# Kernel tuning notes

Measured on AMD Instinct MI355X. Metric: run time of the kernel, lower is better.

## Reference

```python
import jax, jax.numpy as jnp
import numpy as np

D_MODEL = 1024
NHEAD = 16
HEAD_DIM = D_MODEL // NHEAD
D_FF = 4096
B, S = 2, 2048
LN_EPS = 1e-5


def _linear_params(key, d_out, d_in):
    kw, kb = jax.random.split(key)
    lim = 1.0 / np.sqrt(d_in)
    W = jax.random.uniform(kw, (d_out, d_in), jnp.float32, -lim, lim)
    b = jax.random.uniform(kb, (d_out,), jnp.float32, -lim, lim)
    return W, b


def setup_inputs() -> dict:
    key = jax.random.key(0)
    ks = jax.random.split(key, 8)
    src = jax.random.normal(ks[0], (B, S, D_MODEL), jnp.float32)
    mask = jax.random.randint(ks[1], (B, S), 0, 2).astype(bool)
    Wq, bq = _linear_params(ks[2], D_MODEL, D_MODEL)
    Wk, bk = _linear_params(ks[3], D_MODEL, D_MODEL)
    Wv, bv = _linear_params(ks[4], D_MODEL, D_MODEL)
    Wo, bo = _linear_params(ks[5], D_MODEL, D_MODEL)
    W1, b1 = _linear_params(ks[6], D_FF, D_MODEL)
    W2, b2 = _linear_params(ks[7], D_MODEL, D_FF)
    ln1_g = jnp.ones((D_MODEL,), jnp.float32)
    ln1_b = jnp.zeros((D_MODEL,), jnp.float32)
    ln2_g = jnp.ones((D_MODEL,), jnp.float32)
    ln2_b = jnp.zeros((D_MODEL,), jnp.float32)
    return dict(src=src, mask=mask, Wq=Wq, bq=bq, Wk=Wk, bk=bk, Wv=Wv, bv=bv,
                Wo=Wo, bo=bo, W1=W1, b1=b1, W2=W2, b2=b2,
                ln1_g=ln1_g, ln1_b=ln1_b, ln2_g=ln2_g, ln2_b=ln2_b)


def _layernorm(x, g, b):
    mu = jnp.mean(x, axis=-1, keepdims=True)
    var = jnp.mean(jnp.square(x - mu), axis=-1, keepdims=True)
    return (x - mu) * jax.lax.rsqrt(var + LN_EPS) * g + b


def reference(src, mask, Wq, bq, Wk, bk, Wv, bv, Wo, bo, W1, b1, W2, b2,
              ln1_g, ln1_b, ln2_g, ln2_b):
    batch, seq, _ = src.shape
    src_norm = _layernorm(src, ln1_g, ln1_b)
    # projections (torch Linear: x @ W.T + b), split heads -> [B,H,S,Dh]
    def proj(W, b):
        y = jnp.einsum('bsi,oi->bso', src_norm, W) + b
        return y.reshape(batch, seq, NHEAD, HEAD_DIM).transpose(0, 2, 1, 3)
    q, k, v = proj(Wq, bq), proj(Wk, bk), proj(Wv, bv)
    scores = jnp.einsum('bhqd,bhkd->bhqk', q, k) / np.sqrt(HEAD_DIM)
    scores = jnp.where(mask[:, None, None, :], -10000.0, scores)
    attn_probs = jax.nn.softmax(scores, axis=-1)
    attn_out = jnp.einsum('bhqk,bhkd->bhqd', attn_probs, v)
    attn_out = attn_out.transpose(0, 2, 1, 3).reshape(batch, seq, D_MODEL)
    attn_out = jnp.einsum('bsi,oi->bso', attn_out, Wo) + bo
    src = src + attn_out
    src_norm2 = _layernorm(src, ln2_g, ln2_b)
    h = jax.nn.relu(jnp.einsum('bsi,oi->bso', src_norm2, W1) + b1)
    ff = jnp.einsum('bsi,oi->bso', h, W2) + b2
    src = src + ff
    return (src, attn_probs)
```

## Files before the change

### kernel.cpp

```cpp
#include <hip/hip_runtime.h>
#include <math.h>

typedef __bf16 bf16;
typedef __bf16 bf16x4 __attribute__((ext_vector_type(4)));
typedef __bf16 bf16x8 __attribute__((ext_vector_type(8)));
typedef float f32x4 __attribute__((ext_vector_type(4)));

__device__ __forceinline__ f32x4 mfma16(bf16x8 a, bf16x8 b, f32x4 c) {
  return __builtin_amdgcn_mfma_f32_16x16x32_bf16(a, b, c, 0, 0, 0);
}

__device__ __forceinline__ void gload_lds16(const void* g, void* l) {
  __builtin_amdgcn_global_load_lds((__attribute__((address_space(1))) void*)(g),
                                   (__attribute__((address_space(3))) void*)(l),
                                   16, 0, 0);
}

__global__ __launch_bounds__(256)
void cvt_all(const float* __restrict__ Wq, const float* __restrict__ Wk,
             const float* __restrict__ Wv, const float* __restrict__ Wo,
             const float* __restrict__ W1, const float* __restrict__ W2,
             const float* __restrict__ bq, const float* __restrict__ bk,
             const float* __restrict__ bv, bf16* __restrict__ wqkv,
             bf16* __restrict__ wob, bf16* __restrict__ w1b,
             bf16* __restrict__ w2b, float* __restrict__ bqkv) {
  const int i = blockIdx.x * 256 + threadIdx.x;
  if (i < 3145728) {
    float4 v;
    bf16* dst;
    size_t di;
    if (i < 262144) { v = ((const float4*)Wq)[i]; dst = wqkv; di = i; }
    else if (i < 524288) { v = ((const float4*)Wk)[i - 262144]; dst = wqkv; di = i; }
    else if (i < 786432) { v = ((const float4*)Wv)[i - 524288]; dst = wqkv; di = i; }
    else if (i < 1048576) { v = ((const float4*)Wo)[i - 786432]; dst = wob; di = i - 786432; }
    else if (i < 2097152) { v = ((const float4*)W1)[i - 1048576]; dst = w1b; di = i - 1048576; }
    else { v = ((const float4*)W2)[i - 2097152]; dst = w2b; di = i - 2097152; }
    bf16x4 o;
    o[0] = (bf16)v.x; o[1] = (bf16)v.y; o[2] = (bf16)v.z; o[3] = (bf16)v.w;
    reinterpret_cast<bf16x4*>(dst)[di] = o;
  } else {
    const int j = i - 3145728;
    const float* s = (j < 256) ? bq : ((j < 512) ? bk : bv);
    reinterpret_cast<float4*>(bqkv)[j] = reinterpret_cast<const float4*>(s)[j & 255];
  }
}

__global__ __launch_bounds__(256)
void ln_bf16(const float* __restrict__ x, const float* __restrict__ g,
             const float* __restrict__ bta, bf16* __restrict__ y) {
  const int row = blockIdx.x, t = threadIdx.x;
  const float4 v = reinterpret_cast<const float4*>(x)[(size_t)row * 256 + t];
  float s1 = v.x + v.y + v.z + v.w;
  float s2 = v.x * v.x + v.y * v.y + v.z * v.z + v.w * v.w;
#pragma unroll
  for (int m = 1; m < 64; m <<= 1) {
    s1 += __shfl_xor(s1, m);
    s2 += __shfl_xor(s2, m);
  }
  __shared__ float red[8];
  if ((t & 63) == 0) { red[(t >> 6) * 2] = s1; red[(t >> 6) * 2 + 1] = s2; }
  __syncthreads();
  s1 = red[0] + red[2] + red[4] + red[6];
  s2 = red[1] + red[3] + red[5] + red[7];
  const float mu = s1 * (1.f / 1024.f);
  const float rs = rsqrtf(s2 * (1.f / 1024.f) - mu * mu + 1e-5f);
  const float4 gv = reinterpret_cast<const float4*>(g)[t];
  const float4 bv = reinterpret_cast<const float4*>(bta)[t];
  bf16x4 o;
  o[0] = (bf16)((v.x - mu) * rs * gv.x + bv.x);
  o[1] = (bf16)((v.y - mu) * rs * gv.y + bv.y);
  o[2] = (bf16)((v.z - mu) * rs * gv.z + bv.z);
  o[3] = (bf16)((v.w - mu) * rs * gv.w + bv.w);
  reinterpret_cast<bf16x4*>(y)[(size_t)row * 256 + t] = o;
}

__global__ __launch_bounds__(256)
void tr_v(const bf16* __restrict__ QKV, bf16* __restrict__ VT) {
  __shared__ bf16 T[64 * 80];
  const int t = threadIdx.x;
  const int sb = blockIdx.x * 64, h = blockIdx.y, b = blockIdx.z;
  const int srow = t >> 2, c16 = t & 3;
  const bf16* src = QKV + (size_t)(b * 2048 + sb + srow) * 3072 + 2048 + h * 64 + c16 * 16;
  bf16x8 a0 = *reinterpret_cast<const bf16x8*>(src);
  bf16x8 a1 = *reinterpret_cast<const bf16x8*>(src + 8);
  *reinterpret_cast<bf16x8*>(&T[srow * 80 + c16 * 16]) = a0;
  *reinterpret_cast<bf16x8*>(&T[srow * 80 + c16 * 16 + 8]) = a1;
  __syncthreads();
  const int drow = t >> 2, sq = t & 3;
  bf16x8 o0, o1;
#pragma unroll
  for (int j = 0; j < 8; ++j) o0[j] = T[(sq * 16 + j) * 80 + drow];
#pragma unroll
  for (int j = 0; j < 8; ++j) o1[j] = T[(sq * 16 + 8 + j) * 80 + drow];
  bf16* dst = VT + ((size_t)(b * 16 + h) * 64 + drow) * 2048 + sb + sq * 16;
  *reinterpret_cast<bf16x8*>(dst) = o0;
  *reinterpret_cast<bf16x8*>(dst + 8) = o1;
}

template <bool OUT_BF16, bool RELU, bool RES, bool QSC>
__global__ __launch_bounds__(256)
void gemm_bt(const bf16* __restrict__ A, const bf16* __restrict__ Bw,
             const float* __restrict__ bias, const float* __restrict__ res,
             void* __restrict__ Cout, int M, int N, int K) {
  __shared__ bf16 As[2][128 * 32];
  __shared__ bf16 Bs[2][128 * 32];
  const int t = threadIdx.x, wave = t >> 6, lane = t & 63;
  const int l15 = lane & 15, lhi = lane >> 4;
  const int nwg = gridDim.x * gridDim.y;
  const int orig = blockIdx.y * gridDim.x + blockIdx.x;
  const int wgid = (orig & 7) * (nwg >> 3) + (orig >> 3);
  const int bx = wgid % gridDim.x, by = wgid / gridDim.x;
  const int m0 = by * 128, n0 = bx * 128;
  const int wm = (wave >> 1) * 64, wn = (wave & 1) * 64;
  const f32x4 z4 = {0.f, 0.f, 0.f, 0.f};
  f32x4 acc[4][4];
#pragma unroll
  for (int m = 0; m < 4; ++m)
#pragma unroll
    for (int n = 0; n < 4; ++n) acc[m][n] = z4;

  const int soff0 = wave * 1024 + lane * 16;
  const int soff1 = (4 + wave) * 1024 + lane * 16;
  const int srow0 = soff0 >> 6, scol0 = (soff0 & 63) >> 1;
  const int srow1 = soff1 >> 6, scol1 = (soff1 & 63) >> 1;

#define GEMM_STAGE(k0, bb)                                                    \
  do {                                                                        \
    gload_lds16(A + (size_t)(m0 + srow0) * K + (k0) + scol0,                  \
                (char*)As[bb] + soff0);                                       \
    gload_lds16(Bw + (size_t)(n0 + srow0) * K + (k0) + scol0,                 \
                (char*)Bs[bb] + soff0);                                       \
    gload_lds16(A + (size_t)(m0 + srow1) * K + (k0) + scol1,                  \
                (char*)As[bb] + soff1);                                       \
    gload_lds16(Bw + (size_t)(n0 + srow1) * K + (k0) + scol1,                 \
                (char*)Bs[bb] + soff1);                                       \
  } while (0)

  GEMM_STAGE(0, 0);
  asm volatile("s_waitcnt vmcnt(0)" ::: "memory");
  __builtin_amdgcn_s_barrier();

  int cur = 0;
  for (int k0 = 0; k0 < K; k0 += 32) {
    if (k0 + 32 < K) GEMM_STAGE(k0 + 32, cur ^ 1);
    bf16x8 af[4], bfr[4];
#pragma unroll
    for (int m = 0; m < 4; ++m)
      af[m] = *reinterpret_cast<const bf16x8*>(&As[cur][(wm + m * 16 + l15) * 32 + lhi * 8]);
#pragma unroll
    for (int n = 0; n < 4; ++n)
      bfr[n] = *reinterpret_cast<const bf16x8*>(&Bs[cur][(wn + n * 16 + l15) * 32 + lhi * 8]);
    __builtin_amdgcn_s_setprio(1);
#pragma unroll
    for (int m = 0; m < 4; ++m)
#pragma unroll
      for (int n = 0; n < 4; ++n) acc[m][n] = mfma16(af[m], bfr[n], acc[m][n]);
    __builtin_amdgcn_s_setprio(0);
    asm volatile("s_waitcnt vmcnt(0)" ::: "memory");
    __builtin_amdgcn_s_barrier();
    cur ^= 1;
  }
#undef GEMM_STAGE

  const float sc = (QSC && n0 < 1024) ? 0.125f : 1.0f;
#pragma unroll
  for (int m = 0; m < 4; ++m) {
    const int row_base = m0 + wm + m * 16 + lhi * 4;
#pragma unroll
    for (int n = 0; n < 4; ++n) {
      const int col = n0 + wn + n * 16 + l15;
      const float bv = bias[col];
#pragma unroll
      for (int r = 0; r < 4; ++r) {
        const int row = row_base + r;
        float v = (acc[m][n][r] + bv) * sc;
        if (RELU) v = v > 0.f ? v : 0.f;
        if (RES) v += res[(size_t)row * N + col];
        if (OUT_BF16)
          ((bf16*)Cout)[(size_t)row * N + col] = (bf16)v;
        else
          ((float*)Cout)[(size_t)row * N + col] = v;
      }
    }
  }
}

__global__ __launch_bounds__(512)
void attn_fused2(const bf16* __restrict__ Qp, const bf16* __restrict__ Kp,
                 const bf16* __restrict__ VTp, const int* __restrict__ mask,
                 float* __restrict__ probs, bf16* __restrict__ Ob) {
  constexpr int S = 2048, LD = 3072, KB = 128, NT = S / KB;
  __shared__ bf16 Kt[KB * 64];
  __shared__ bf16 Vt[64 * KB];
  __shared__ bf16 P[128 * KB];
  __shared__ float msk[KB];
  const int t = threadIdx.x, wave = t >> 6, lane = t & 63;
  const int l15 = lane & 15, lhi = lane >> 4;
  const int flat = blockIdx.x + 16 * (blockIdx.y + 16 * blockIdx.z);
  const int wg = (flat & 7) * 64 + (flat >> 3);
  const int q0 = (wg & 15) * 128, h = (wg >> 4) & 15, b = wg >> 8;
  const int* mrow = mask + b * S;
  const f32x4 z4 = {0.f, 0.f, 0.f, 0.f};

  const bf16* kgp[2];
  const bf16* vgp[2];
  int soff[2];
#pragma unroll
  for (int i = 0; i < 2; ++i) {
    const int off = (i * 8 + wave) * 1024 + lane * 16;
    soff[i] = off;
    const int krow = off >> 7, kbin = off & 127;
    kgp[i] = Kp + (size_t)(b * S + krow) * LD + h * 64 + ((kbin ^ ((krow & 7) << 4)) >> 1);
    const int d = off >> 8, vbin = off & 255;
    vgp[i] = VTp + (size_t)((b * 16 + h) * 64 + d) * S + ((vbin ^ ((d & 7) << 4)) >> 1);
  }

  bf16x8 qf[2];
#pragma unroll
  for (int ks = 0; ks < 2; ++ks)
    qf[ks] = *reinterpret_cast<const bf16x8*>(
        Qp + (size_t)(b * S + q0 + wave * 16 + l15) * LD + h * 64 + ks * 32 + lhi * 8);

  bf16x8 kreg[2];
  float mnext;
#pragma unroll
  for (int i = 0; i < 2; ++i) kreg[i] = *reinterpret_cast<const bf16x8*>(kgp[i]);
  mnext = (t < KB) ? (mrow[t] ? 0.f : 1.f) : 0.f;
#pragma unroll
  for (int i = 0; i < 2; ++i)
    *reinterpret_cast<bf16x8*>((char*)Kt + soff[i]) = kreg[i];
  if (t < KB) msk[t] = mnext;
  __syncthreads();

  float lpart = 0.f;
  for (int kt = 0; kt < NT; ++kt) {
    const int kv0 = kt * KB;
    if (kt + 1 < NT) {
#pragma unroll
      for (int i = 0; i < 2; ++i)
        kreg[i] = *reinterpret_cast<const bf16x8*>(kgp[i] + (size_t)(kv0 + KB) * LD);
      mnext = (t < KB) ? (mrow[kv0 + KB + t] ? 0.f : 1.f) : 0.f;
    }
    f32x4 sa[8];
#pragma unroll
    for (int n = 0; n < 8; ++n) sa[n] = z4;
    __builtin_amdgcn_s_setprio(1);
#pragma unroll
    for (int ks = 0; ks < 2; ++ks)
#pragma unroll
      for (int n = 0; n < 8; ++n) {
        const int krow = n * 16 + l15;
        bf16x8 kf = *reinterpret_cast<const bf16x8*>(
            (char*)Kt + krow * 128 + ((ks * 64 + lhi * 16) ^ ((krow & 7) << 4)));
        sa[n] = mfma16(kf, qf[ks], sa[n]);
      }
    __builtin_amdgcn_s_setprio(0);
#pragma unroll
    for (int n = 0; n < 8; ++n)
#pragma unroll
      for (int r = 0; r < 4; ++r)
        lpart += __expf(sa[n][r] - 15.f) * msk[n * 16 + lhi * 4 + r];
    __syncthreads();
    if (kt + 1 < NT) {
#pragma unroll
      for (int i = 0; i < 2; ++i)
        *reinterpret_cast<bf16x8*>((char*)Kt + soff[i]) = kreg[i];
      if (t < KB) msk[t] = mnext;
    }
    __syncthreads();
  }
  lpart += __shfl_xor(lpart, 16);
  lpart += __shfl_xor(lpart, 32);
  const float il = 1.f / lpart;

  f32x4 oa[4];
#pragma unroll
  for (int n = 0; n < 4; ++n) oa[n] = z4;
  float* pbase = probs + ((size_t)(b * 16 + h) * S + q0 + wave * 16 + l15) * S;
  const int prw = wave * 16 + l15;

  bf16x8 vreg[2];
#pragma unroll
  for (int i = 0; i < 2; ++i) {
    kreg[i] = *reinterpret_cast<const bf16x8*>(kgp[i]);
    vreg[i] = *reinterpret_cast<const bf16x8*>(vgp[i]);
  }
  mnext = (t < KB) ? (mrow[t] ? 0.f : 1.f) : 0.f;
#pragma unroll
  for (int i = 0; i < 2; ++i) {
    *reinterpret_cast<bf16x8*>((char*)Kt + soff[i]) = kreg[i];
    *reinterpret_cast<bf16x8*>((char*)Vt + soff[i]) = vreg[i];
  }
  if (t < KB) msk[t] = mnext;
  __syncthreads();

  for (int kt = 0; kt < NT; ++kt) {
    const int kv0 = kt * KB;
    if (kt + 1 < NT) {
#pragma unroll
      for (int i = 0; i < 2; ++i) {
        kreg[i] = *reinterpret_cast<const bf16x8*>(kgp[i] + (size_t)(kv0 + KB) * LD);
        vreg[i] = *reinterpret_cast<const bf16x8*>(vgp[i] + kv0 + KB);
      }
      mnext = (t < KB) ? (mrow[kv0 + KB + t] ? 0.f : 1.f) : 0.f;
    }

    f32x4 sa[8];
#pragma unroll
    for (int n = 0; n < 8; ++n) sa[n] = z4;
    __builtin_amdgcn_s_setprio(1);
#pragma unroll
    for (int ks = 0; ks < 2; ++ks)
#pragma unroll
      for (int n = 0; n < 8; ++n) {
        const int krow = n * 16 + l15;
        bf16x8 kf = *reinterpret_cast<const bf16x8*>(
            (char*)Kt + krow * 128 + ((ks * 64 + lhi * 16) ^ ((krow & 7) << 4)));
        sa[n] = mfma16(kf, qf[ks], sa[n]);
      }
    __builtin_amdgcn_s_setprio(0);

#pragma unroll
    for (int n = 0; n < 8; ++n) {
      f32x4 pn;
#pragma unroll
      for (int r = 0; r < 4; ++r)
        pn[r] = __expf(sa[n][r] - 15.f) * msk[n * 16 + lhi * 4 + r] * il;
      *reinterpret_cast<f32x4*>(pbase + kv0 + n * 16 + lhi * 4) = pn;
      bf16x4 pb;
      pb[0] = (bf16)pn[0]; pb[1] = (bf16)pn[1];
      pb[2] = (bf16)pn[2]; pb[3] = (bf16)pn[3];
      *reinterpret_cast<bf16x4*>(
          (char*)P + prw * 256 + ((n * 32 + lhi * 8) ^ ((prw & 7) << 4))) = pb;
    }
    __builtin_amdgcn_s_setprio(1);
#pragma unroll
    for (int ks = 0; ks < 4; ++ks) {
      bf16x8 pf = *reinterpret_cast<const bf16x8*>(
          (char*)P + prw * 256 + ((ks * 64 + lhi * 16) ^ ((prw & 7) << 4)));
#pragma unroll
      for (int nn = 0; nn < 4; ++nn) {
        const int vr = nn * 16 + l15;
        bf16x8 vf = *reinterpret_cast<const bf16x8*>(
            (char*)Vt + vr * 256 + ((ks * 64 + lhi * 16) ^ ((vr & 7) << 4)));
        oa[nn] = mfma16(pf, vf, oa[nn]);
      }
    }
    __builtin_amdgcn_s_setprio(0);
    __syncthreads();
    if (kt + 1 < NT) {
#pragma unroll
      for (int i = 0; i < 2; ++i) {
        *reinterpret_cast<bf16x8*>((char*)Kt + soff[i]) = kreg[i];
        *reinterpret_cast<bf16x8*>((char*)Vt + soff[i]) = vreg[i];
      }
      if (t < KB) msk[t] = mnext;
    }
    __syncthreads();
  }

#pragma unroll
  for (int nn = 0; nn < 4; ++nn)
#pragma unroll
    for (int r = 0; r < 4; ++r)
      Ob[(size_t)(b * S + q0 + wave * 16 + lhi * 4 + r) * 1024 + h * 64 + nn * 16 + l15] =
          (bf16)oa[nn][r];
}

extern "C" void kernel_launch(void* const* d_in, const int* in_sizes, int n_in,
                              void* d_out, int out_size, void* d_ws, size_t ws_size,
                              hipStream_t stream) {
  const float* src = (const float*)d_in[0];
  const int* mask = (const int*)d_in[1];
  const float* Wq = (const float*)d_in[2];
  const float* bq = (const float*)d_in[3];
  const float* Wk = (const float*)d_in[4];
  const float* bk = (const float*)d_in[5];
  const float* Wv = (const float*)d_in[6];
  const float* bv = (const float*)d_in[7];
  const float* Wo = (const float*)d_in[8];
  const float* bo = (const float*)d_in[9];
  const float* W1 = (const float*)d_in[10];
  const float* b1 = (const float*)d_in[11];
  const float* W2 = (const float*)d_in[12];
  const float* b2 = (const float*)d_in[13];
  const float* ln1g = (const float*)d_in[14];
  const float* ln1b = (const float*)d_in[15];
  const float* ln2g = (const float*)d_in[16];
  const float* ln2b = (const float*)d_in[17];

  float* out0 = (float*)d_out;
  float* probs = (float*)d_out + (size_t)4194304;

  char* w = (char*)d_ws;
  const size_t MB = 1u << 20;
  bf16* wqkv = (bf16*)(w);
  bf16* wob = (bf16*)(w + 6 * MB);
  bf16* w1b = (bf16*)(w + 8 * MB);
  bf16* w2b = (bf16*)(w + 16 * MB);
  bf16* xn = (bf16*)(w + 24 * MB);
  bf16* QKV = (bf16*)(w + 32 * MB);
  bf16* Ob = (bf16*)(w + 56 * MB);
  bf16* hb = (bf16*)(w + 32 * MB);
  bf16* VT = (bf16*)(w + 64 * MB);
  float* s2 = (float*)(w + 64 * MB);
  float* bqkv = (float*)(w + 80 * MB);

  cvt_all<<<12291, 256, 0, stream>>>(Wq, Wk, Wv, Wo, W1, W2, bq, bk, bv,
                                     wqkv, wob, w1b, w2b, bqkv);

  ln_bf16<<<4096, 256, 0, stream>>>(src, ln1g, ln1b, xn);
  gemm_bt<true, false, false, true><<<dim3(24, 32), 256, 0, stream>>>(
      xn, wqkv, bqkv, nullptr, QKV, 4096, 3072, 1024);
  tr_v<<<dim3(32, 16, 2), 256, 0, stream>>>(QKV, VT);
  attn_fused2<<<dim3(16, 16, 2), 512, 0, stream>>>(
      QKV, QKV + 1024, VT, mask, probs, Ob);
  gemm_bt<false, false, true, false><<<dim3(8, 32), 256, 0, stream>>>(
      Ob, wob, bo, src, s2, 4096, 1024, 1024);
  ln_bf16<<<4096, 256, 0, stream>>>(s2, ln2g, ln2b, xn);
  gemm_bt<true, true, false, false><<<dim3(32, 32), 256, 0, stream>>>(
      xn, w1b, b1, nullptr, hb, 4096, 4096, 1024);
  gemm_bt<false, false, true, false><<<dim3(8, 32), 256, 0, stream>>>(
      hb, w2b, b2, s2, out0, 4096, 1024, 4096);

  (void)in_sizes; (void)n_in; (void)out_size; (void)ws_size;
}
```

Measured before the change: 451.2 us.

## Triple-buffer GEMM LDS stages and double-buffer K in attention row-sum pass

The GEMM main loop moves from a two-stage to a three-stage LDS ring, prefetching two k-tiles ahead and waiting with vmcnt(4) so one tile's loads stay in flight across the barrier. In the attention kernel's first (row-sum) pass, K tiles now ping-pong between the Kt and Vt buffers, which are free at that point, and the mask gets a double buffer. This removes one of the two __syncthreads per iteration. The cost is more LDS per GEMM block (possibly lower occupancy) and a more delicate waitcnt accounting.

Result: faster. 434.8 us (-3.6%).

```diff
diff --git a/kernel.cpp b/kernel.cpp
--- a/kernel.cpp
+++ b/kernel.cpp
@@ -102,8 +102,8 @@
 void gemm_bt(const bf16* __restrict__ A, const bf16* __restrict__ Bw,
              const float* __restrict__ bias, const float* __restrict__ res,
              void* __restrict__ Cout, int M, int N, int K) {
-  __shared__ bf16 As[2][128 * 32];
-  __shared__ bf16 Bs[2][128 * 32];
+  __shared__ bf16 As[3][128 * 32];
+  __shared__ bf16 Bs[3][128 * 32];
   const int t = threadIdx.x, wave = t >> 6, lane = t & 63;
   const int l15 = lane & 15, lhi = lane >> 4;
   const int nwg = gridDim.x * gridDim.y;
@@ -136,29 +136,36 @@
                 (char*)Bs[bb] + soff1);                                       \
   } while (0)
 
+  const int nt = K >> 5;
   GEMM_STAGE(0, 0);
-  asm volatile("s_waitcnt vmcnt(0)" ::: "memory");
+  GEMM_STAGE(32, 1);
+  asm volatile("s_waitcnt vmcnt(4)" ::: "memory");
   __builtin_amdgcn_s_barrier();
 
-  int cur = 0;
-  for (int k0 = 0; k0 < K; k0 += 32) {
-    if (k0 + 32 < K) GEMM_STAGE(k0 + 32, cur ^ 1);
+  for (int kt = 0; kt < nt; ++kt) {
+    if (kt + 2 < nt) GEMM_STAGE((kt + 2) * 32, (kt + 2) % 3);
+    const bf16* Ac = As[kt % 3];
+    const bf16* Bc = Bs[kt % 3];
     bf16x8 af[4], bfr[4];
 #pragma unroll
     for (int m = 0; m < 4; ++m)
-      af[m] = *reinterpret_cast<const bf16x8*>(&As[cur][(wm + m * 16 + l15) * 32 + lhi * 8]);
+      af[m] = *reinterpret_cast<const bf16x8*>(&Ac[(wm + m * 16 + l15) * 32 + lhi * 8]);
 #pragma unroll
     for (int n = 0; n < 4; ++n)
-      bfr[n] = *reinterpret_cast<const bf16x8*>(&Bs[cur][(wn + n * 16 + l15) * 32 + lhi * 8]);
+      bfr[n] = *reinterpret_cast<const bf16x8*>(&Bc[(wn + n * 16 + l15) * 32 + lhi * 8]);
     __builtin_amdgcn_s_setprio(1);
 #pragma unroll
     for (int m = 0; m < 4; ++m)
 #pragma unroll
       for (int n = 0; n < 4; ++n) acc[m][n] = mfma16(af[m], bfr[n], acc[m][n]);
     __builtin_amdgcn_s_setprio(0);
-    asm volatile("s_waitcnt vmcnt(0)" ::: "memory");
-    __builtin_amdgcn_s_barrier();
-    cur ^= 1;
+    if (kt + 1 < nt) {
+      if (kt + 2 < nt)
+        asm volatile("s_waitcnt vmcnt(4)" ::: "memory");
+      else
+        asm volatile("s_waitcnt vmcnt(0)" ::: "memory");
+      __builtin_amdgcn_s_barrier();
+    }
   }
 #undef GEMM_STAGE
 
@@ -193,7 +200,7 @@
   __shared__ bf16 Kt[KB * 64];
   __shared__ bf16 Vt[64 * KB];
   __shared__ bf16 P[128 * KB];
-  __shared__ float msk[KB];
+  __shared__ float msk2[2][KB];
   const int t = threadIdx.x, wave = t >> 6, lane = t & 63;
   const int l15 = lane & 15, lhi = lane >> 4;
   const int flat = blockIdx.x + 16 * (blockIdx.y + 16 * blockIdx.z);
@@ -229,7 +236,7 @@
 #pragma unroll
   for (int i = 0; i < 2; ++i)
     *reinterpret_cast<bf16x8*>((char*)Kt + soff[i]) = kreg[i];
-  if (t < KB) msk[t] = mnext;
+  if (t < KB) msk2[0][t] = mnext;
   __syncthreads();
 
   float lpart = 0.f;
@@ -241,6 +248,72 @@
         kreg[i] = *reinterpret_cast<const bf16x8*>(kgp[i] + (size_t)(kv0 + KB) * LD);
       mnext = (t < KB) ? (mrow[kv0 + KB + t] ? 0.f : 1.f) : 0.f;
     }
+    const char* kb = (kt & 1) ? (const char*)Vt : (const char*)Kt;
+    const float* mc = msk2[kt & 1];
+    f32x4 sa[8];
+#pragma unroll
+    for (int n = 0; n < 8; ++n) sa[n] = z4;
+    __builtin_amdgcn_s_setprio(1);
+#pragma unroll
+    for (int ks = 0; ks < 2; ++ks)
+#pragma unroll
+      for (int n = 0; n < 8; ++n) {
+        const int krow = n * 16 + l15;
+        bf16x8 kf = *reinterpret_cast<const bf16x8*>(
+            kb + krow * 128 + ((ks * 64 + lhi * 16) ^ ((krow & 7) << 4)));
+        sa[n] = mfma16(kf, qf[ks], sa[n]);
+      }
+    __builtin_amdgcn_s_setprio(0);
+#pragma unroll
+    for (int n = 0; n < 8; ++n)
+#pragma unroll
+      for (int r = 0; r < 4; ++r)
+        lpart += __expf(sa[n][r] - 15.f) * mc[n * 16 + lhi * 4 + r];
+    if (kt + 1 < NT) {
+      char* kbn = ((kt + 1) & 1) ? (char*)Vt : (char*)Kt;
+#pragma unroll
+      for (int i = 0; i < 2; ++i)
+        *reinterpret_cast<bf16x8*>(kbn + soff[i]) = kreg[i];
+      if (t < KB) msk2[(kt + 1) & 1][t] = mnext;
+    }
+    __syncthreads();
+  }
+  lpart += __shfl_xor(lpart, 16);
+  lpart += __shfl_xor(lpart, 32);
+  const float il = 1.f / lpart;
+
+  f32x4 oa[4];
+#pragma unroll
+  for (int n = 0; n < 4; ++n) oa[n] = z4;
+  float* pbase = probs + ((size_t)(b * 16 + h) * S + q0 + wave * 16 + l15) * S;
+  const int prw = wave * 16 + l15;
+
+  bf16x8 vreg[2];
+#pragma unroll
+  for (int i = 0; i < 2; ++i) {
+    kreg[i] = *reinterpret_cast<const bf16x8*>(kgp[i]);
+    vreg[i] = *reinterpret_cast<const bf16x8*>(vgp[i]);
+  }
+  mnext = (t < KB) ? (mrow[t] ? 0.f : 1.f) : 0.f;
+#pragma unroll
+  for (int i = 0; i < 2; ++i) {
+    *reinterpret_cast<bf16x8*>((char*)Kt + soff[i]) = kreg[i];
+    *reinterpret_cast<bf16x8*>((char*)Vt + soff[i]) = vreg[i];
+  }
+  if (t < KB) msk2[0][t] = mnext;
+  __syncthreads();
+
+  for (int kt = 0; kt < NT; ++kt) {
+    const int kv0 = kt * KB;
+    if (kt + 1 < NT) {
+#pragma unroll
+      for (int i = 0; i < 2; ++i) {
+        kreg[i] = *reinterpret_cast<const bf16x8*>(kgp[i] + (size_t)(kv0 + KB) * LD);
+        vreg[i] = *reinterpret_cast<const bf16x8*>(vgp[i] + kv0 + KB);
+      }
+      mnext = (t < KB) ? (mrow[kv0 + KB + t] ? 0.f : 1.f) : 0.f;
+    }
+
     f32x4 sa[8];
 #pragma unroll
     for (int n = 0; n < 8; ++n) sa[n] = z4;
@@ -255,77 +328,13 @@
         sa[n] = mfma16(kf, qf[ks], sa[n]);
       }
     __builtin_amdgcn_s_setprio(0);
-#pragma unroll
-    for (int n = 0; n < 8; ++n)
-#pragma unroll
-      for (int r = 0; r < 4; ++r)
-        lpart += __expf(sa[n][r] - 15.f) * msk[n * 16 + lhi * 4 + r];
-    __syncthreads();
-    if (kt + 1 < NT) {
-#pragma unroll
-      for (int i = 0; i < 2; ++i)
-        *reinterpret_cast<bf16x8*>((char*)Kt + soff[i]) = kreg[i];
-      if (t < KB) msk[t] = mnext;
-    }
-    __syncthreads();
-  }
-  lpart += __shfl_xor(lpart, 16);
-  lpart += __shfl_xor(lpart, 32);
-  const float il = 1.f / lpart;
-
-  f32x4 oa[4];
-#pragma unroll
-  for (int n = 0; n < 4; ++n) oa[n] = z4;
-  float* pbase = probs + ((size_t)(b * 16 + h) * S + q0 + wave * 16 + l15) * S;
-  const int prw = wave * 16 + l15;
-
-  bf16x8 vreg[2];
-#pragma unroll
-  for (int i = 0; i < 2; ++i) {
-    kreg[i] = *reinterpret_cast<const bf16x8*>(kgp[i]);
-    vreg[i] = *reinterpret_cast<const bf16x8*>(vgp[i]);
-  }
-  mnext = (t < KB) ? (mrow[t] ? 0.f : 1.f) : 0.f;
-#pragma unroll
-  for (int i = 0; i < 2; ++i) {
-    *reinterpret_cast<bf16x8*>((char*)Kt + soff[i]) = kreg[i];
-    *reinterpret_cast<bf16x8*>((char*)Vt + soff[i]) = vreg[i];
-  }
-  if (t < KB) msk[t] = mnext;
-  __syncthreads();
-
-  for (int kt = 0; kt < NT; ++kt) {
-    const int kv0 = kt * KB;
-    if (kt + 1 < NT) {
-#pragma unroll
-      for (int i = 0; i < 2; ++i) {
-        kreg[i] = *reinterpret_cast<const bf16x8*>(kgp[i] + (size_t)(kv0 + KB) * LD);
-        vreg[i] = *reinterpret_cast<const bf16x8*>(vgp[i] + kv0 + KB);
-      }
-      mnext = (t < KB) ? (mrow[kv0 + KB + t] ? 0.f : 1.f) : 0.f;
-    }
-
-    f32x4 sa[8];
-#pragma unroll
-    for (int n = 0; n < 8; ++n) sa[n] = z4;
-    __builtin_amdgcn_s_setprio(1);
-#pragma unroll
-    for (int ks = 0; ks < 2; ++ks)
-#pragma unroll
-      for (int n = 0; n < 8; ++n) {
-        const int krow = n * 16 + l15;
-        bf16x8 kf = *reinterpret_cast<const bf16x8*>(
-            (char*)Kt + krow * 128 + ((ks * 64 + lhi * 16) ^ ((krow & 7) << 4)));
-        sa[n] = mfma16(kf, qf[ks], sa[n]);
-      }
-    __builtin_amdgcn_s_setprio(0);
 
 #pragma unroll
     for (int n = 0; n < 8; ++n) {
       f32x4 pn;
 #pragma unroll
       for (int r = 0; r < 4; ++r)
-        pn[r] = __expf(sa[n][r] - 15.f) * msk[n * 16 + lhi * 4 + r] * il;
+        pn[r] = __expf(sa[n][r] - 15.f) * msk2[0][n * 16 + lhi * 4 + r] * il;
       *reinterpret_cast<f32x4*>(pbase + kv0 + n * 16 + lhi * 4) = pn;
       bf16x4 pb;
       pb[0] = (bf16)pn[0]; pb[1] = (bf16)pn[1];
@@ -354,7 +363,7 @@
         *reinterpret_cast<bf16x8*>((char*)Kt + soff[i]) = kreg[i];
         *reinterpret_cast<bf16x8*>((char*)Vt + soff[i]) = vreg[i];
       }
-      if (t < KB) msk[t] = mnext;
+      if (t < KB) msk2[0][t] = mnext;
     }
     __syncthreads();
   }
```
